# Kernel optimization log

Measured on AMD Instinct MI355X. Metric: run time of the kernel, lower is better.

## Reference

```python
import jax, jax.numpy as jnp
import numpy as np


def setup_inputs() -> dict:
    key = jax.random.key(0)
    ks = jax.random.split(key, 5)
    B, T, I, H = 64, 2048, 128, 128
    bound = 1.0 / np.sqrt(H)
    x = jax.random.normal(ks[0], (B, T, I), dtype=jnp.float32)
    W_xh = jax.random.uniform(ks[1], (H, I), minval=-bound, maxval=bound, dtype=jnp.float32)
    b_xh = jax.random.uniform(ks[2], (H,), minval=-bound, maxval=bound, dtype=jnp.float32)
    W_hh = jax.random.uniform(ks[3], (H, H), minval=-bound, maxval=bound, dtype=jnp.float32)
    b_hh = jax.random.uniform(ks[4], (H,), minval=-bound, maxval=bound, dtype=jnp.float32)
    return {"x": x, "W_xh": W_xh, "b_xh": b_xh, "W_hh": W_hh, "b_hh": b_hh}


def reference(x, W_xh, b_xh, W_hh, b_hh):
    # x: [B, T, I]; nn.Linear applies x @ W.T + b.
    # Precompute the input projection for all timesteps in one GEMM.
    xp = jnp.einsum('bti,hi->bth', x, W_xh) + b_xh  # [B, T, H]
    B = x.shape[0]
    H = W_hh.shape[0]
    h0 = jnp.zeros((B, H), dtype=x.dtype)

    def step(h, xt):
        h_new = jnp.tanh(xt + h @ W_hh.T + b_hh)
        return h_new, h_new

    h_last, hs = jax.lax.scan(step, h0, jnp.swapaxes(xp, 0, 1))  # hs: [T, B, H]
    h_seq = jnp.swapaxes(hs, 0, 1)  # [B, T, H]
    return h_seq, h_last[None]  # h: [1, B, H]
```

## Files before the change

kernel.cpp:

```cpp
#include <hip/hip_runtime.h>

#define B_ 64
#define T_ 2048
#define I_ 128
#define H_ 128
#define CHUNK 128
#define NCHUNK (T_ / CHUNK)

__global__ __launch_bounds__(256) void xp_gemm(
    const float* __restrict__ x, const float* __restrict__ Wxh,
    const float* __restrict__ bxh, float* __restrict__ xp)
{
    __shared__ float ws[H_ * I_];
    const int tid = threadIdx.x;
    {
        const float4* src = (const float4*)Wxh;
        float4* dst = (float4*)ws;
        #pragma unroll
        for (int i = 0; i < (H_ * I_ / 4) / 256; ++i)
            dst[tid + i * 256] = src[tid + i * 256];
    }
    __syncthreads();

    const int r  = tid & 127;
    const int ch = tid >> 7;
    const long row = (long)blockIdx.x * 128 + r;
    const float* xrow = x + row * I_;
    const float* wb = ws + ch * 64 * I_;

    float acc[64];
    #pragma unroll
    for (int c = 0; c < 64; ++c) acc[c] = 0.f;

    for (int k4 = 0; k4 < I_ / 4; ++k4) {
        const float4 xv = *(const float4*)(xrow + k4 * 4);
        #pragma unroll
        for (int c = 0; c < 64; ++c) {
            const float4 wv = *(const float4*)(wb + c * I_ + k4 * 4);
            acc[c] = fmaf(xv.x, wv.x, acc[c]);
            acc[c] = fmaf(xv.y, wv.y, acc[c]);
            acc[c] = fmaf(xv.z, wv.z, acc[c]);
            acc[c] = fmaf(xv.w, wv.w, acc[c]);
        }
    }

    float* orow = xp + row * H_ + ch * 64;
    const float4* bv = (const float4*)(bxh + ch * 64);
    #pragma unroll
    for (int c4 = 0; c4 < 16; ++c4) {
        const float4 b4 = bv[c4];
        float4 o;
        o.x = acc[c4 * 4 + 0] + b4.x;
        o.y = acc[c4 * 4 + 1] + b4.y;
        o.z = acc[c4 * 4 + 2] + b4.z;
        o.w = acc[c4 * 4 + 3] + b4.w;
        *(float4*)(orow + c4 * 4) = o;
    }
}

__device__ __forceinline__ void stage_chunk(const float* __restrict__ g,
                                            float* l, int wv, int ln)
{
    #pragma unroll
    for (int i = 0; i < 16; ++i) {
        const int off = i * 1024 + wv * 256;
        __builtin_amdgcn_global_load_lds(
            (const __attribute__((address_space(1))) unsigned int*)(g + off + ln * 4),
            (__attribute__((address_space(3))) unsigned int*)(l + off),
            16, 0, 0);
    }
}

__global__ __launch_bounds__(256, 1) void rnn_scan(
    const float* __restrict__ Whh, const float* __restrict__ bhh,
    float* __restrict__ seq , float* __restrict__ hlast)
{
    __shared__ float xpl[2][CHUNK * H_];
    __shared__ float hb[2][136];

    const int tid  = threadIdx.x;
    const int j    = tid >> 1;
    const int half = tid & 1;
    const int b    = blockIdx.x;
    const int wv   = tid >> 6;
    const int ln   = tid & 63;

    float w[64];
    {
        const float* wr = Whh + j * H_ + half * 64;
        #pragma unroll
        for (int i4 = 0; i4 < 16; ++i4) {
            const float4 v = *(const float4*)(wr + i4 * 4);
            w[i4 * 4 + 0] = v.x; w[i4 * 4 + 1] = v.y;
            w[i4 * 4 + 2] = v.z; w[i4 * 4 + 3] = v.w;
        }
    }
    const float bj = bhh[j];
    if (tid < 136) { hb[0][tid] = 0.f; hb[1][tid] = 0.f; }

    float* xp = seq + (size_t)b * T_ * H_;

    stage_chunk(xp, &xpl[0][0], wv, ln);

    const int slot = j + ((j >> 6) << 2);
    int cur = 0;
    for (int c = 0; c < NCHUNK; ++c) {
        asm volatile("s_waitcnt vmcnt(0)" ::: "memory");
        __syncthreads();
        if (c + 1 < NCHUNK)
            stage_chunk(xp + (size_t)(c + 1) * CHUNK * H_, &xpl[(c + 1) & 1][0], wv, ln);

        const float* xb = &xpl[c & 1][0];
        float* sq = xp + (size_t)c * CHUNK * H_;

        for (int t = 0; t < CHUNK; ++t) {
            const float xcur = xb[t * H_ + j];
            const float* hc = &hb[cur][half * 68];
            float a0 = 0.f, a1 = 0.f, a2 = 0.f, a3 = 0.f;
            #pragma unroll
            for (int i4 = 0; i4 < 16; ++i4) {
                const float4 hv = *(const float4*)(hc + i4 * 4);
                a0 = fmaf(hv.x, w[i4 * 4 + 0], a0);
                a1 = fmaf(hv.y, w[i4 * 4 + 1], a1);
                a2 = fmaf(hv.z, w[i4 * 4 + 2], a2);
                a3 = fmaf(hv.w, w[i4 * 4 + 3], a3);
            }
            float s = (a0 + a1) + (a2 + a3);
            s += __shfl_xor(s, 1);
            const float pre = xcur + bj + s;
            const float e = exp2f(pre * 2.8853900817779268f);
            const float hnew = 1.f - 2.f * __builtin_amdgcn_rcpf(e + 1.f);
            if (!half) {
                hb[cur ^ 1][slot] = hnew;
                sq[t * H_ + j] = hnew;
            }
            asm volatile("s_waitcnt lgkmcnt(0)" ::: "memory");
            __builtin_amdgcn_s_barrier();
            cur ^= 1;
        }
    }
    if (!half) hlast[b * H_ + j] = hb[cur][slot];
}

extern "C" void kernel_launch(void* const* d_in, const int* in_sizes, int n_in,
                              void* d_out, int out_size, void* d_ws, size_t ws_size,
                              hipStream_t stream)
{
    const float* x   = (const float*)d_in[0];
    const float* Wxh = (const float*)d_in[1];
    const float* bxh = (const float*)d_in[2];
    const float* Whh = (const float*)d_in[3];
    const float* bhh = (const float*)d_in[4];
    float* out   = (float*)d_out;
    float* hlast = out + (size_t)B_ * T_ * H_;

    xp_gemm<<<(B_ * T_) / 128, 256, 0, stream>>>(x, Wxh, bxh, out);
    rnn_scan<<<B_, 256, 0, stream>>>(Whh, bhh, out, hlast);
}
```

Measured before the change: 1.172 ms.

## Run recurrence in one wavefront with fp16 dot2, retile input GEMM

The recurrent scan now uses a single 64-lane wavefront per batch row. Each lane computes two hidden units with packed fp16 weights and hidden state through v_dot2 instructions, and the per-step workgroup barrier is removed. The input-projection GEMM is retiled to 8x8 register blocks with double-buffered operand loads. The goal is to cut barrier and LDS latency on the sequential critical path and raise arithmetic density in the GEMM. In exchange, fp16 rounding of weights and hidden state across 2048 steps adds error that may exceed tolerance, and the barrier-free single-wave handoff relies on wave-level lockstep semantics.

```diff
diff --git a/kernel.cpp b/kernel.cpp
--- a/kernel.cpp
+++ b/kernel.cpp
@@ -7,6 +7,25 @@
 #define CHUNK 128
 #define NCHUNK (T_ / CHUNK)
 
+typedef _Float16 half2v __attribute__((ext_vector_type(2)));
+
+__device__ __forceinline__ float fdot2(unsigned h, unsigned w, float acc) {
+#if __has_builtin(__builtin_amdgcn_fdot2)
+    return __builtin_amdgcn_fdot2(__builtin_bit_cast(half2v, h),
+                                  __builtin_bit_cast(half2v, w), acc, false);
+#else
+    half2v a = __builtin_bit_cast(half2v, h);
+    half2v b = __builtin_bit_cast(half2v, w);
+    acc = fmaf((float)a.x, (float)b.x, acc);
+    return fmaf((float)a.y, (float)b.y, acc);
+#endif
+}
+
+__device__ __forceinline__ unsigned pkh(float a, float b) {
+    half2v v; v.x = (_Float16)a; v.y = (_Float16)b;
+    return __builtin_bit_cast(unsigned, v);
+}
+
 __global__ __launch_bounds__(256) void xp_gemm(
     const float* __restrict__ x, const float* __restrict__ Wxh,
     const float* __restrict__ bxh, float* __restrict__ xp)
@@ -22,48 +41,75 @@
     }
     __syncthreads();
 
-    const int r  = tid & 127;
-    const int ch = tid >> 7;
-    const long row = (long)blockIdx.x * 128 + r;
-    const float* xrow = x + row * I_;
-    const float* wb = ws + ch * 64 * I_;
-
-    float acc[64];
-    #pragma unroll
-    for (int c = 0; c < 64; ++c) acc[c] = 0.f;
-
-    for (int k4 = 0; k4 < I_ / 4; ++k4) {
-        const float4 xv = *(const float4*)(xrow + k4 * 4);
-        #pragma unroll
-        for (int c = 0; c < 64; ++c) {
-            const float4 wv = *(const float4*)(wb + c * I_ + k4 * 4);
-            acc[c] = fmaf(xv.x, wv.x, acc[c]);
-            acc[c] = fmaf(xv.y, wv.y, acc[c]);
-            acc[c] = fmaf(xv.z, wv.z, acc[c]);
-            acc[c] = fmaf(xv.w, wv.w, acc[c]);
+    const int r0 = (tid >> 4) * 8;
+    const int c0 = (tid & 15) * 8;
+    const float* xb = x + ((size_t)blockIdx.x * 128 + r0) * I_;
+    const float* wb = ws + c0 * I_;
+
+    float acc[8][8];
+    #pragma unroll
+    for (int i = 0; i < 8; ++i)
+        #pragma unroll
+        for (int j = 0; j < 8; ++j) acc[i][j] = 0.f;
+
+    float4 xa[8], wa[8], xn[8], wn[8];
+    #pragma unroll
+    for (int i = 0; i < 8; ++i) xa[i] = *(const float4*)(xb + i * I_);
+    #pragma unroll
+    for (int j = 0; j < 8; ++j) wa[j] = *(const float4*)(wb + j * I_);
+
+    for (int k4 = 0; k4 < 32; k4 += 2) {
+        #pragma unroll
+        for (int i = 0; i < 8; ++i) xn[i] = *(const float4*)(xb + i * I_ + k4 * 4 + 4);
+        #pragma unroll
+        for (int j = 0; j < 8; ++j) wn[j] = *(const float4*)(wb + j * I_ + k4 * 4 + 4);
+        #pragma unroll
+        for (int i = 0; i < 8; ++i)
+            #pragma unroll
+            for (int j = 0; j < 8; ++j) {
+                acc[i][j] = fmaf(xa[i].x, wa[j].x, acc[i][j]);
+                acc[i][j] = fmaf(xa[i].y, wa[j].y, acc[i][j]);
+                acc[i][j] = fmaf(xa[i].z, wa[j].z, acc[i][j]);
+                acc[i][j] = fmaf(xa[i].w, wa[j].w, acc[i][j]);
+            }
+        if (k4 + 2 < 32) {
+            #pragma unroll
+            for (int i = 0; i < 8; ++i) xa[i] = *(const float4*)(xb + i * I_ + k4 * 4 + 8);
+            #pragma unroll
+            for (int j = 0; j < 8; ++j) wa[j] = *(const float4*)(wb + j * I_ + k4 * 4 + 8);
         }
-    }
-
-    float* orow = xp + row * H_ + ch * 64;
-    const float4* bv = (const float4*)(bxh + ch * 64);
-    #pragma unroll
-    for (int c4 = 0; c4 < 16; ++c4) {
-        const float4 b4 = bv[c4];
-        float4 o;
-        o.x = acc[c4 * 4 + 0] + b4.x;
-        o.y = acc[c4 * 4 + 1] + b4.y;
-        o.z = acc[c4 * 4 + 2] + b4.z;
-        o.w = acc[c4 * 4 + 3] + b4.w;
-        *(float4*)(orow + c4 * 4) = o;
-    }
-}
-
-__device__ __forceinline__ void stage_chunk(const float* __restrict__ g,
-                                            float* l, int wv, int ln)
-{
-    #pragma unroll
-    for (int i = 0; i < 16; ++i) {
-        const int off = i * 1024 + wv * 256;
+        #pragma unroll
+        for (int i = 0; i < 8; ++i)
+            #pragma unroll
+            for (int j = 0; j < 8; ++j) {
+                acc[i][j] = fmaf(xn[i].x, wn[j].x, acc[i][j]);
+                acc[i][j] = fmaf(xn[i].y, wn[j].y, acc[i][j]);
+                acc[i][j] = fmaf(xn[i].z, wn[j].z, acc[i][j]);
+                acc[i][j] = fmaf(xn[i].w, wn[j].w, acc[i][j]);
+            }
+    }
+
+    const float4 b0 = *(const float4*)(bxh + c0);
+    const float4 b1 = *(const float4*)(bxh + c0 + 4);
+    float* orow = xp + ((size_t)blockIdx.x * 128 + r0) * H_ + c0;
+    #pragma unroll
+    for (int i = 0; i < 8; ++i) {
+        float4 o0, o1;
+        o0.x = acc[i][0] + b0.x; o0.y = acc[i][1] + b0.y;
+        o0.z = acc[i][2] + b0.z; o0.w = acc[i][3] + b0.w;
+        o1.x = acc[i][4] + b1.x; o1.y = acc[i][5] + b1.y;
+        o1.z = acc[i][6] + b1.z; o1.w = acc[i][7] + b1.w;
+        *(float4*)(orow + i * H_) = o0;
+        *(float4*)(orow + i * H_ + 4) = o1;
+    }
+}
+
+__device__ __forceinline__ void stage_chunk64(const float* __restrict__ g,
+                                              float* l, int ln)
+{
+    #pragma unroll
+    for (int i = 0; i < 64; ++i) {
+        const int off = i * 256;
         __builtin_amdgcn_global_load_lds(
             (const __attribute__((address_space(1))) unsigned int*)(g + off + ln * 4),
             (__attribute__((address_space(3))) unsigned int*)(l + off),
@@ -71,75 +117,71 @@
     }
 }
 
-__global__ __launch_bounds__(256, 1) void rnn_scan(
+__global__ __launch_bounds__(64, 1) void rnn_scan(
     const float* __restrict__ Whh, const float* __restrict__ bhh,
     float* __restrict__ seq , float* __restrict__ hlast)
 {
     __shared__ float xpl[2][CHUNK * H_];
-    __shared__ float hb[2][136];
-
-    const int tid  = threadIdx.x;
-    const int j    = tid >> 1;
-    const int half = tid & 1;
-    const int b    = blockIdx.x;
-    const int wv   = tid >> 6;
-    const int ln   = tid & 63;
-
-    float w[64];
-    {
-        const float* wr = Whh + j * H_ + half * 64;
-        #pragma unroll
-        for (int i4 = 0; i4 < 16; ++i4) {
-            const float4 v = *(const float4*)(wr + i4 * 4);
-            w[i4 * 4 + 0] = v.x; w[i4 * 4 + 1] = v.y;
-            w[i4 * 4 + 2] = v.z; w[i4 * 4 + 3] = v.w;
-        }
-    }
-    const float bj = bhh[j];
-    if (tid < 136) { hb[0][tid] = 0.f; hb[1][tid] = 0.f; }
+    __shared__ unsigned hpk[2][64];
+
+    const int l  = threadIdx.x;
+    const int b  = blockIdx.x;
+    const int j0 = 2 * l;
+
+    unsigned w0[64], w1[64];
+    #pragma unroll
+    for (int i = 0; i < 64; ++i) {
+        const float2 a = *(const float2*)&Whh[(size_t)j0 * H_ + 2 * i];
+        const float2 c = *(const float2*)&Whh[(size_t)(j0 + 1) * H_ + 2 * i];
+        w0[i] = pkh(a.x, a.y);
+        w1[i] = pkh(c.x, c.y);
+    }
+    const float bj0 = bhh[j0], bj1 = bhh[j0 + 1];
+    hpk[0][l] = 0u;
+    hpk[1][l] = 0u;
 
     float* xp = seq + (size_t)b * T_ * H_;
-
-    stage_chunk(xp, &xpl[0][0], wv, ln);
-
-    const int slot = j + ((j >> 6) << 2);
-    int cur = 0;
+    stage_chunk64(xp, &xpl[0][0], l);
+
+    float h0 = 0.f, h1 = 0.f;
+    int tg = 0;
     for (int c = 0; c < NCHUNK; ++c) {
         asm volatile("s_waitcnt vmcnt(0)" ::: "memory");
-        __syncthreads();
         if (c + 1 < NCHUNK)
-            stage_chunk(xp + (size_t)(c + 1) * CHUNK * H_, &xpl[(c + 1) & 1][0], wv, ln);
+            stage_chunk64(xp + (size_t)(c + 1) * CHUNK * H_, &xpl[(c + 1) & 1][0], l);
 
         const float* xb = &xpl[c & 1][0];
         float* sq = xp + (size_t)c * CHUNK * H_;
 
-        for (int t = 0; t < CHUNK; ++t) {
-            const float xcur = xb[t * H_ + j];
-            const float* hc = &hb[cur][half * 68];
-            float a0 = 0.f, a1 = 0.f, a2 = 0.f, a3 = 0.f;
-            #pragma unroll
-            for (int i4 = 0; i4 < 16; ++i4) {
-                const float4 hv = *(const float4*)(hc + i4 * 4);
-                a0 = fmaf(hv.x, w[i4 * 4 + 0], a0);
-                a1 = fmaf(hv.y, w[i4 * 4 + 1], a1);
-                a2 = fmaf(hv.z, w[i4 * 4 + 2], a2);
-                a3 = fmaf(hv.w, w[i4 * 4 + 3], a3);
+        for (int t = 0; t < CHUNK; ++t, ++tg) {
+            const int cur = tg & 1;
+            const uint4* hb = (const uint4*)&hpk[cur][0];
+            float a00 = bj0, a01 = 0.f, a10 = bj1, a11 = 0.f;
+            #pragma unroll
+            for (int i = 0; i < 16; ++i) {
+                const uint4 hv = hb[i];
+                a00 = fdot2(hv.x, w0[4 * i + 0], a00);
+                a01 = fdot2(hv.y, w0[4 * i + 1], a01);
+                a00 = fdot2(hv.z, w0[4 * i + 2], a00);
+                a01 = fdot2(hv.w, w0[4 * i + 3], a01);
+                a10 = fdot2(hv.x, w1[4 * i + 0], a10);
+                a11 = fdot2(hv.y, w1[4 * i + 1], a11);
+                a10 = fdot2(hv.z, w1[4 * i + 2], a10);
+                a11 = fdot2(hv.w, w1[4 * i + 3], a11);
             }
-            float s = (a0 + a1) + (a2 + a3);
-            s += __shfl_xor(s, 1);
-            const float pre = xcur + bj + s;
-            const float e = exp2f(pre * 2.8853900817779268f);
-            const float hnew = 1.f - 2.f * __builtin_amdgcn_rcpf(e + 1.f);
-            if (!half) {
-                hb[cur ^ 1][slot] = hnew;
-                sq[t * H_ + j] = hnew;
-            }
+            const float2 xc = *(const float2*)&xb[t * H_ + j0];
+            const float p0 = xc.x + a00 + a01;
+            const float p1 = xc.y + a10 + a11;
+            const float e0 = exp2f(p0 * 2.8853900817779268f);
+            const float e1 = exp2f(p1 * 2.8853900817779268f);
+            h0 = 1.f - 2.f * __builtin_amdgcn_rcpf(e0 + 1.f);
+            h1 = 1.f - 2.f * __builtin_amdgcn_rcpf(e1 + 1.f);
+            *(float2*)&sq[t * H_ + j0] = make_float2(h0, h1);
+            hpk[cur ^ 1][l] = pkh(h0, h1);
             asm volatile("s_waitcnt lgkmcnt(0)" ::: "memory");
-            __builtin_amdgcn_s_barrier();
-            cur ^= 1;
         }
     }
-    if (!half) hlast[b * H_ + j] = hb[cur][slot];
+    *(float2*)&hlast[b * H_ + j0] = make_float2(h0, h1);
 }
 
 extern "C" void kernel_launch(void* const* d_in, const int* in_sizes, int n_in,
@@ -155,5 +197,5 @@
     float* hlast = out + (size_t)B_ * T_ * H_;
 
     xp_gemm<<<(B_ * T_) / 128, 256, 0, stream>>>(x, Wxh, bxh, out);
-    rnn_scan<<<B_, 256, 0, stream>>>(Whh, bhh, out, hlast);
-}
+    rnn_scan<<<B_, 64, 0, stream>>>(Whh, bhh, out, hlast);
+}
```

New measurement: 1.788 ms. +52.6%, slower.
